# Performance work log

Measured on AMD Instinct MI355X. Metric: run time of the kernel, lower is better.

Reference implementation:

```python
import jax, jax.numpy as jnp
import numpy as np

DIM = 1024
N_HEAD = 16
N_KV_HEAD = 4
HEAD_DIM = DIM // N_HEAD  # 64
INTER = 2688
B, N = 2, 2048
EPS = 1e-6


def setup_inputs() -> dict:
    key = jax.random.key(0)
    ks = jax.random.split(key, 10)
    std = 0.02
    x = jax.random.normal(ks[0], (B, N, DIM), dtype=jnp.float32)
    # rotary embedding: theta = pos * 10000^(-2i/d), cos/sin of shape [N, HEAD_DIM//2]
    inv_freq = 1.0 / (10000.0 ** (np.arange(0, HEAD_DIM, 2, dtype=np.float32) / HEAD_DIM))
    t = np.arange(N, dtype=np.float32)
    ang = np.outer(t, inv_freq)  # [N, HEAD_DIM//2]
    rope_cos = jnp.asarray(np.cos(ang))
    rope_sin = jnp.asarray(np.sin(ang))
    mask = jnp.tril(jnp.ones((N, N), dtype=bool))  # True = attend
    return {
        "x": x,
        "w_attn_norm": jnp.ones((DIM,), jnp.float32),
        "w_ffn_norm": jnp.ones((DIM,), jnp.float32),
        "Wq": jax.random.normal(ks[1], (DIM, N_HEAD * HEAD_DIM), jnp.float32) * std,
        "Wkv": jax.random.normal(ks[2], (DIM, 2 * N_KV_HEAD * HEAD_DIM), jnp.float32) * std,
        "Wo": jax.random.normal(ks[3], (N_HEAD * HEAD_DIM, DIM), jnp.float32) * std,
        "W1": jax.random.normal(ks[4], (DIM, INTER), jnp.float32) * std,
        "W2": jax.random.normal(ks[5], (INTER, DIM), jnp.float32) * std,
        "W3": jax.random.normal(ks[6], (DIM, INTER), jnp.float32) * std,
        "rope_cos": rope_cos,
        "rope_sin": rope_sin,
        "mask": mask,
    }


def _rms_norm(x, w):
    # nn.functional.rms_norm: x / sqrt(mean(x^2) + eps) * w
    return x * jax.lax.rsqrt(jnp.mean(x * x, axis=-1, keepdims=True) + EPS) * w


def _apply_rope(x, cos, sin):
    # x: [b, n, h, d]; consecutive pairs (x[2k], x[2k+1]) form complex numbers
    xr = x[..., 0::2]
    xi = x[..., 1::2]
    c = cos[None, :, None, :]
    s = sin[None, :, None, :]
    yr = xr * c - xi * s
    yi = xr * s + xi * c
    return jnp.stack([yr, yi], axis=-1).reshape(x.shape)


def _block(x, w_attn_norm, w_ffn_norm, Wq, Wkv, Wo, W1, W2, W3, rope_cos, rope_sin, mask):
    b, n, _ = x.shape
    # --- attention (GQA, use_cache=False prefill) ---
    h = _rms_norm(x, w_attn_norm)
    q = (h @ Wq).reshape(b, n, N_HEAD, HEAD_DIM)
    kv = h @ Wkv
    k, v = jnp.split(kv, 2, axis=-1)
    k = k.reshape(b, n, N_KV_HEAD, HEAD_DIM)
    v = v.reshape(b, n, N_KV_HEAD, HEAD_DIM)
    q = _apply_rope(q, rope_cos, rope_sin)
    k = _apply_rope(k, rope_cos, rope_sin)
    # einops repeat 'b n h d -> b n (r h) d' == tile along head axis
    r = N_HEAD // N_KV_HEAD
    k = jnp.tile(k, (1, 1, r, 1))
    v = jnp.tile(v, (1, 1, r, 1))
    scale = HEAD_DIM ** -0.5
    scores = jnp.einsum('bnhd,bmhd->bhnm', q, k) * scale
    scores = jnp.where(mask[None, None, :, :], scores, jnp.finfo(scores.dtype).min)
    attn = jax.nn.softmax(scores, axis=-1)
    o = jnp.einsum('bhnm,bmhd->bnhd', attn, v).reshape(b, n, N_HEAD * HEAD_DIM)
    x = x + o @ Wo
    # --- SwiGLU MLP ---
    h2 = _rms_norm(x, w_ffn_norm)
    ff = (jax.nn.silu(h2 @ W1) * (h2 @ W3)) @ W2
    return x + ff


def reference(x, w_attn_norm, w_ffn_norm, Wq, Wkv, Wo, W1, W2, W3, rope_cos, rope_sin, mask):
    return _block(x, w_attn_norm, w_ffn_norm, Wq, Wkv, Wo, W1, W2, W3, rope_cos, rope_sin, mask)
```

## Files before the change

### kernel.cpp

```cpp
#include <hip/hip_runtime.h>

#define DIM 1024
#define NH 16
#define NKV 4
#define HD 64
#define INTER 2688
#define BB 2
#define NN 2048
#define MM (BB*NN)

typedef __attribute__((ext_vector_type(4))) float f32x4;
typedef __attribute__((ext_vector_type(16))) float f32x16;
typedef __attribute__((ext_vector_type(8))) short short8;

#define CROW(r,h) ((((r)&3)) + 8*((r)>>2) + 4*(h))

__device__ __forceinline__ unsigned short f2bf(float f) {
  union { float f; unsigned u; } v; v.f = f;
  unsigned r = v.u + 0x7fffu + ((v.u >> 16) & 1u);
  return (unsigned short)(r >> 16);
}
__device__ __forceinline__ float bf2f(unsigned short u) {
  union { unsigned u; float f; } v; v.u = ((unsigned)u) << 16; return v.f;
}
__device__ __forceinline__ float ld_res(const float* p) { return *p; }
__device__ __forceinline__ float ld_res(const unsigned short* p) { return bf2f(*p); }
__device__ __forceinline__ void st_out(float* p, float v) { *p = v; }
__device__ __forceinline__ void st_out(unsigned short* p, float v) { *p = f2bf(v); }

__device__ __forceinline__ void glds16(const unsigned short* g, unsigned short* l) {
  __builtin_amdgcn_global_load_lds(
      (const __attribute__((address_space(1))) void*)g,
      (__attribute__((address_space(3))) void*)l, 16, 0, 0);
}

__device__ __forceinline__ void xcd_map(int& bx, int& by) {
  int gx = gridDim.x;
  int nwg = gx * gridDim.y;
  int bid = (int)blockIdx.y * gx + (int)blockIdx.x;
  int cpx = nwg >> 3;
  int lg = (bid & 7) * cpx + (bid >> 3);
  bx = lg % gx;
  by = lg / gx;
}

__global__ void transpose_all(const float* __restrict__ Wq, const float* __restrict__ Wkv,
                              const float* __restrict__ Wo, const float* __restrict__ W1,
                              const float* __restrict__ W3, const float* __restrict__ W2,
                              unsigned short* __restrict__ WqkvT, unsigned short* __restrict__ WoT,
                              unsigned short* __restrict__ W1T, unsigned short* __restrict__ W3T,
                              unsigned short* __restrict__ W2T) {
  int tb = blockIdx.x;
  const float* src; unsigned short* dst; int K, Nc, t0;
  if (tb < 1024)        { src = Wq;  dst = WqkvT;                         K = 1024; Nc = 1024; t0 = tb; }
  else if (tb < 1536)   { src = Wkv; dst = WqkvT + (size_t)1024 * 1024;   K = 1024; Nc = 512;  t0 = tb - 1024; }
  else if (tb < 2560)   { src = Wo;  dst = WoT;                           K = 1024; Nc = 1024; t0 = tb - 1536; }
  else if (tb < 5248)   { src = W1;  dst = W1T;                           K = 1024; Nc = 2688; t0 = tb - 2560; }
  else if (tb < 7936)   { src = W3;  dst = W3T;                           K = 1024; Nc = 2688; t0 = tb - 5248; }
  else                  { src = W2;  dst = W2T;                           K = 2688; Nc = 1024; t0 = tb - 7936; }
  int ntx = Nc >> 5;
  int n0 = (t0 % ntx) * 32, k0 = (t0 / ntx) * 32;
  __shared__ float tile[32][33];
  int tx = threadIdx.x & 31, ty = threadIdx.x >> 5;
#pragma unroll
  for (int i = 0; i < 32; i += 8)
    tile[ty + i][tx] = src[(size_t)(k0 + ty + i) * Nc + n0 + tx];
  __syncthreads();
#pragma unroll
  for (int i = 0; i < 32; i += 8)
    dst[(size_t)(n0 + ty + i) * K + k0 + tx] = f2bf(tile[tx][ty + i]);
}

template <typename InT>
__global__ void rmsnorm_k(const InT* __restrict__ x, const float* __restrict__ w,
                          unsigned short* __restrict__ h) {
  int row = blockIdx.x;
  int t = threadIdx.x;
  float4 v;
  if constexpr (sizeof(InT) == 4) {
    v = ((const float4*)(x + (size_t)row * DIM))[t];
  } else {
    ushort4 u = ((const ushort4*)(x + (size_t)row * DIM))[t];
    v.x = bf2f(u.x); v.y = bf2f(u.y); v.z = bf2f(u.z); v.w = bf2f(u.w);
  }
  float ss = v.x * v.x + v.y * v.y + v.z * v.z + v.w * v.w;
#pragma unroll
  for (int o = 1; o < 64; o <<= 1) ss += __shfl_xor(ss, o);
  __shared__ float ps[4];
  if ((t & 63) == 0) ps[t >> 6] = ss;
  __syncthreads();
  float r = rsqrtf((ps[0] + ps[1] + ps[2] + ps[3]) * (1.0f / DIM) + 1e-6f);
  float4 wv = ((const float4*)w)[t];
  ushort4 o4;
  o4.x = f2bf(v.x * r * wv.x);
  o4.y = f2bf(v.y * r * wv.y);
  o4.z = f2bf(v.z * r * wv.z);
  o4.w = f2bf(v.w * r * wv.w);
  *(ushort4*)(h + (size_t)row * DIM + t * 4) = o4;
}

template <typename ResT, typename OutT>
__global__ __launch_bounds__(256, 3) void gemm64(
    const unsigned short* __restrict__ A, const unsigned short* __restrict__ Bt,
    const ResT* __restrict__ res, OutT* __restrict__ C, int Nc, int K) {
  __shared__ __align__(16) unsigned short Asm[2][64 * 64];
  __shared__ __align__(16) unsigned short Bsm[2][128 * 64];
  int tid = threadIdx.x;
  int w = tid >> 6, l = tid & 63;
  int bx, by;
  xcd_map(bx, by);
  int bm = by * 64, bn = bx * 128;
  int wc = w * 32;
  int c0 = l & 15, g = l >> 4;

  int sra = w * 16 + (l >> 3);
  int srb = w * 32 + (l >> 3);
  int schA = ((l & 7) ^ (l >> 3)) * 8;
  const unsigned short* gA = A + (size_t)(bm + sra) * K + schA;
  const unsigned short* gB = Bt + (size_t)(bn + srb) * K + schA;
  int lsa = (w * 16) * 64, lsb = (w * 32) * 64;

  f32x4 acc[4][2] = {};
  int T = K / 64;
  glds16(gA, &Asm[0][lsa]);
  glds16(gA + 8 * K, &Asm[0][lsa + 8 * 64]);
  glds16(gB, &Bsm[0][lsb]);
  glds16(gB + 8 * K, &Bsm[0][lsb + 8 * 64]);
  glds16(gB + 16 * K, &Bsm[0][lsb + 16 * 64]);
  glds16(gB + 24 * K, &Bsm[0][lsb + 24 * 64]);
  __syncthreads();
  int buf = 0;
  for (int s = 0; s < T; ++s) {
    int nb = buf ^ 1;
    if (s + 1 < T) {
      int ko = (s + 1) * 64;
      glds16(gA + ko, &Asm[nb][lsa]);
      glds16(gA + 8 * K + ko, &Asm[nb][lsa + 8 * 64]);
      glds16(gB + ko, &Bsm[nb][lsb]);
      glds16(gB + 8 * K + ko, &Bsm[nb][lsb + 8 * 64]);
      glds16(gB + 16 * K + ko, &Bsm[nb][lsb + 16 * 64]);
      glds16(gB + 24 * K + ko, &Bsm[nb][lsb + 24 * 64]);
    }
    const unsigned short* As = Asm[buf];
    const unsigned short* Bs = Bsm[buf];
#pragma unroll
    for (int ks = 0; ks < 2; ++ks) {
      short8 af[4], bf[2];
#pragma unroll
      for (int m = 0; m < 4; m++) {
        int ra = m * 16 + c0;
        af[m] = *(const short8*)&As[ra * 64 + (((ks * 4 + g) ^ (ra & 7)) * 8)];
      }
#pragma unroll
      for (int n = 0; n < 2; n++) {
        int rb = wc + n * 16 + c0;
        bf[n] = *(const short8*)&Bs[rb * 64 + (((ks * 4 + g) ^ (rb & 7)) * 8)];
      }
      __builtin_amdgcn_s_setprio(1);
#pragma unroll
      for (int m = 0; m < 4; m++)
#pragma unroll
        for (int n = 0; n < 2; n++)
          acc[m][n] = __builtin_amdgcn_mfma_f32_16x16x32_bf16(af[m], bf[n], acc[m][n], 0, 0, 0);
      __builtin_amdgcn_s_setprio(0);
    }
    __syncthreads();
    buf = nb;
  }
  int gq = l >> 4;
#pragma unroll
  for (int m = 0; m < 4; m++) {
#pragma unroll
    for (int i = 0; i < 4; i++) {
      int row = bm + m * 16 + gq * 4 + i;
#pragma unroll
      for (int n = 0; n < 2; n++) {
        int col = bn + wc + n * 16 + c0;
        float v = acc[m][n][i] + ld_res(&res[(size_t)row * Nc + col]);
        st_out(&C[(size_t)row * Nc + col], v);
      }
    }
  }
}

__global__ __launch_bounds__(256, 3) void gemm_qkv(
    const unsigned short* __restrict__ A, const unsigned short* __restrict__ Bt,
    const float* __restrict__ cosb, const float* __restrict__ sinb,
    unsigned short* __restrict__ qb, unsigned short* __restrict__ kb,
    unsigned short* __restrict__ vtb) {
  const int K = 1024;
  const float QS = 0.125f * 1.44269504f;
  __shared__ __align__(16) unsigned short Asm[2][64 * 64];
  __shared__ __align__(16) unsigned short Bsm[2][128 * 64];
  int tid = threadIdx.x;
  int w = tid >> 6, l = tid & 63;
  int bx, by;
  xcd_map(bx, by);
  int bm = by * 64, bn = bx * 128;
  int wc = w * 32;
  int c0 = l & 15, g = l >> 4;

  int sra = w * 16 + (l >> 3);
  int srb = w * 32 + (l >> 3);
  int schA = ((l & 7) ^ (l >> 3)) * 8;
  const unsigned short* gA = A + (size_t)(bm + sra) * K + schA;
  const unsigned short* gB = Bt + (size_t)(bn + srb) * K + schA;
  int lsa = (w * 16) * 64, lsb = (w * 32) * 64;

  f32x4 acc[4][2] = {};
  int T = K / 64;
  glds16(gA, &Asm[0][lsa]);
  glds16(gA + 8 * K, &Asm[0][lsa + 8 * 64]);
  glds16(gB, &Bsm[0][lsb]);
  glds16(gB + 8 * K, &Bsm[0][lsb + 8 * 64]);
  glds16(gB + 16 * K, &Bsm[0][lsb + 16 * 64]);
  glds16(gB + 24 * K, &Bsm[0][lsb + 24 * 64]);
  __syncthreads();
  int buf = 0;
  for (int s = 0; s < T; ++s) {
    int nb = buf ^ 1;
    if (s + 1 < T) {
      int ko = (s + 1) * 64;
      glds16(gA + ko, &Asm[nb][lsa]);
      glds16(gA + 8 * K + ko, &Asm[nb][lsa + 8 * 64]);
      glds16(gB + ko, &Bsm[nb][lsb]);
      glds16(gB + 8 * K + ko, &Bsm[nb][lsb + 8 * 64]);
      glds16(gB + 16 * K + ko, &Bsm[nb][lsb + 16 * 64]);
      glds16(gB + 24 * K + ko, &Bsm[nb][lsb + 24 * 64]);
    }
    const unsigned short* As = Asm[buf];
    const unsigned short* Bs = Bsm[buf];
#pragma unroll
    for (int ks = 0; ks < 2; ++ks) {
      short8 af[4], bf[2];
#pragma unroll
      for (int m = 0; m < 4; m++) {
        int ra = m * 16 + c0;
        af[m] = *(const short8*)&As[ra * 64 + (((ks * 4 + g) ^ (ra & 7)) * 8)];
      }
#pragma unroll
      for (int n = 0; n < 2; n++) {
        int rb = wc + n * 16 + c0;
        bf[n] = *(const short8*)&Bs[rb * 64 + (((ks * 4 + g) ^ (rb & 7)) * 8)];
      }
      __builtin_amdgcn_s_setprio(1);
#pragma unroll
      for (int m = 0; m < 4; m++)
#pragma unroll
        for (int n = 0; n < 2; n++)
          acc[m][n] = __builtin_amdgcn_mfma_f32_16x16x32_bf16(af[m], bf[n], acc[m][n], 0, 0, 0);
      __builtin_amdgcn_s_setprio(0);
    }
    __syncthreads();
    buf = nb;
  }
  int gq = l >> 4;
  int lodd = c0 & 1;
#pragma unroll
  for (int m = 0; m < 4; m++) {
#pragma unroll
    for (int i = 0; i < 4; i++) {
      int row = bm + m * 16 + gq * 4 + i;
      int b = row >> 11, tok = row & (NN - 1);
#pragma unroll
      for (int n = 0; n < 2; n++) {
        int col = bn + wc + n * 16 + c0;
        float val = acc[m][n][i];
        float partner = __shfl_xor(val, 1);
        if (bn < 1024) {
          int head = col >> 6, d = col & 63, j = d >> 1;
          float c = cosb[tok * 32 + j], s = sinb[tok * 32 + j];
          float r = lodd ? (partner * s + val * c) : (val * c - partner * s);
          qb[(((size_t)(b * NH + head)) * NN + tok) * 64 + d] = f2bf(r * QS);
        } else if (bn < 1280) {
          int cc = col - 1024;
          int kvh = cc >> 6, d = cc & 63, j = d >> 1;
          float c = cosb[tok * 32 + j], s = sinb[tok * 32 + j];
          float r = lodd ? (partner * s + val * c) : (val * c - partner * s);
          kb[(((size_t)(b * NKV + kvh)) * NN + tok) * 64 + d] = f2bf(r);
        } else {
          int cc = col - 1280;
          int kvh = cc >> 6, d = cc & 63;
          vtb[(((size_t)(b * NKV + kvh)) * 64 + d) * NN + tok] = f2bf(val);
        }
      }
    }
  }
}

__global__ __launch_bounds__(512, 2) void gemm_ffn13(
    const unsigned short* __restrict__ A, const unsigned short* __restrict__ B1t,
    const unsigned short* __restrict__ B3t, unsigned short* __restrict__ G,
    int Nc, int K) {
  __shared__ __align__(16) unsigned short Asm[3][128 * 64];
  __shared__ __align__(16) unsigned short B1sm[3][128 * 64];
  __shared__ __align__(16) unsigned short B3sm[3][128 * 64];
  int tid = threadIdx.x;
  int w = tid >> 6, l = tid & 63;
  int bid = (int)blockIdx.x;
  int xcd = bid & 7, r = bid >> 3;
  int bx = r >> 2, by = (xcd << 2) + (r & 3);
  int bm = by * 128, bn = bx * 128;
  int wm = w >> 2, wn = w & 3;
  int c0 = l & 15, g = l >> 4;

  int lr = l >> 3;
  int sch = ((l & 7) ^ lr) * 8;
  const unsigned short* gA  = A   + (size_t)(bm + w * 16 + lr) * K + sch;
  const unsigned short* gB1 = B1t + (size_t)(bn + w * 16 + lr) * K + sch;
  const unsigned short* gB3 = B3t + (size_t)(bn + w * 16 + lr) * K + sch;
  int ls = (w * 16) * 64;

  f32x4 a1[4][2] = {};
  f32x4 a3[4][2] = {};
  const int T = K / 64;

#pragma unroll
  for (int p = 0; p < 2; ++p) {
    int ko = p * 64;
    glds16(gA + ko, &Asm[p][ls]);
    glds16(gA + 8 * K + ko, &Asm[p][ls + 512]);
    glds16(gB1 + ko, &B1sm[p][ls]);
    glds16(gB1 + 8 * K + ko, &B1sm[p][ls + 512]);
    glds16(gB3 + ko, &B3sm[p][ls]);
    glds16(gB3 + 8 * K + ko, &B3sm[p][ls + 512]);
  }
  asm volatile("s_waitcnt vmcnt(6)" ::: "memory");
  asm volatile("s_barrier" ::: "memory");

  int cur = 0;
  for (int t = 0; t < T; ++t) {
    int nx = cur + 2; if (nx >= 3) nx -= 3;
    bool pre = (t + 2 < T);
    int ko = (t + 2) * 64;
    const unsigned short* As  = Asm[cur];
    const unsigned short* B1s = B1sm[cur];
    const unsigned short* B3s = B3sm[cur];
    short8 af[4], bf[2];

#pragma unroll
    for (int m = 0; m < 4; m++) {
      int ra = wm * 64 + m * 16 + c0;
      af[m] = *(const short8*)&As[ra * 64 + ((g ^ (ra & 7)) * 8)];
    }
#pragma unroll
    for (int n = 0; n < 2; n++) {
      int rb = wn * 32 + n * 16 + c0;
      bf[n] = *(const short8*)&B1s[rb * 64 + ((g ^ (rb & 7)) * 8)];
    }
    if (pre) { glds16(gA + ko, &Asm[nx][ls]); glds16(gA + 8 * K + ko, &Asm[nx][ls + 512]); }
    asm volatile("s_barrier" ::: "memory");
    asm volatile("s_waitcnt lgkmcnt(0)" ::: "memory");
    __builtin_amdgcn_sched_barrier(0);
    __builtin_amdgcn_s_setprio(1);
#pragma unroll
    for (int m = 0; m < 4; m++)
#pragma unroll
      for (int n = 0; n < 2; n++)
        a1[m][n] = __builtin_amdgcn_mfma_f32_16x16x32_bf16(af[m], bf[n], a1[m][n], 0, 0, 0);
    __builtin_amdgcn_s_setprio(0);

#pragma unroll
    for (int n = 0; n < 2; n++) {
      int rb = wn * 32 + n * 16 + c0;
      bf[n] = *(const short8*)&B3s[rb * 64 + ((g ^ (rb & 7)) * 8)];
    }
    if (pre) { glds16(gB1 + ko, &B1sm[nx][ls]); glds16(gB1 + 8 * K + ko, &B1sm[nx][ls + 512]); }
    asm volatile("s_barrier" ::: "memory");
    asm volatile("s_waitcnt lgkmcnt(0)" ::: "memory");
    __builtin_amdgcn_sched_barrier(0);
    __builtin_amdgcn_s_setprio(1);
#pragma unroll
    for (int m = 0; m < 4; m++)
#pragma unroll
      for (int n = 0; n < 2; n++)
        a3[m][n] = __builtin_amdgcn_mfma_f32_16x16x32_bf16(af[m], bf[n], a3[m][n], 0, 0, 0);
    __builtin_amdgcn_s_setprio(0);

#pragma unroll
    for (int m = 0; m < 4; m++) {
      int ra = wm * 64 + m * 16 + c0;
      af[m] = *(const short8*)&As[ra * 64 + (((4 + g) ^ (ra & 7)) * 8)];
    }
#pragma unroll
    for (int n = 0; n < 2; n++) {
      int rb = wn * 32 + n * 16 + c0;
      bf[n] = *(const short8*)&B1s[rb * 64 + (((4 + g) ^ (rb & 7)) * 8)];
    }
    if (pre) { glds16(gB3 + ko, &B3sm[nx][ls]); glds16(gB3 + 8 * K + ko, &B3sm[nx][ls + 512]); }
    asm volatile("s_barrier" ::: "memory");
    asm volatile("s_waitcnt lgkmcnt(0)" ::: "memory");
    __builtin_amdgcn_sched_barrier(0);
    __builtin_amdgcn_s_setprio(1);
#pragma unroll
    for (int m = 0; m < 4; m++)
#pragma unroll
      for (int n = 0; n < 2; n++)
        a1[m][n] = __builtin_amdgcn_mfma_f32_16x16x32_bf16(af[m], bf[n], a1[m][n], 0, 0, 0);
    __builtin_amdgcn_s_setprio(0);

#pragma unroll
    for (int n = 0; n < 2; n++) {
      int rb = wn * 32 + n * 16 + c0;
      bf[n] = *(const short8*)&B3s[rb * 64 + (((4 + g) ^ (rb & 7)) * 8)];
    }
    asm volatile("s_barrier" ::: "memory");
    asm volatile("s_waitcnt lgkmcnt(0)" ::: "memory");
    __builtin_amdgcn_sched_barrier(0);
    __builtin_amdgcn_s_setprio(1);
#pragma unroll
    for (int m = 0; m < 4; m++)
#pragma unroll
      for (int n = 0; n < 2; n++)
        a3[m][n] = __builtin_amdgcn_mfma_f32_16x16x32_bf16(af[m], bf[n], a3[m][n], 0, 0, 0);
    __builtin_amdgcn_s_setprio(0);

    if (pre) {
      asm volatile("s_waitcnt vmcnt(6)" ::: "memory");
    } else if (t + 2 == T) {
      asm volatile("s_waitcnt vmcnt(0)" ::: "memory");
    }
    if (t + 1 < T) asm volatile("s_barrier" ::: "memory");
    cur = cur + 1 == 3 ? 0 : cur + 1;
  }

  int gq = l >> 4;
#pragma unroll
  for (int m = 0; m < 4; m++) {
#pragma unroll
    for (int i = 0; i < 4; i++) {
      int row = bm + wm * 64 + m * 16 + gq * 4 + i;
#pragma unroll
      for (int n = 0; n < 2; n++) {
        int col = bn + wn * 32 + n * 16 + c0;
        float x1 = a1[m][n][i], x3 = a3[m][n][i];
        float sg = x1 / (1.0f + __expf(-x1));
        G[(size_t)row * Nc + col] = f2bf(sg * x3);
      }
    }
  }
}

__global__ __launch_bounds__(256, 3) void attn_k(
    const unsigned short* __restrict__ qg_, const unsigned short* __restrict__ kg_,
    const unsigned short* __restrict__ vg_, unsigned short* __restrict__ ob) {
  __shared__ __align__(16) unsigned short Ksm[2][64 * 64];
  __shared__ __align__(16) unsigned short Vsm[2][64 * 64];
  int qb = (blockIdx.z == 0) ? (int)blockIdx.x : ((int)gridDim.x - 1 - (int)blockIdx.x);
  int h = blockIdx.y, b = blockIdx.z;
  int kvh = h & 3;
  int tid = threadIdx.x, w = tid >> 6, l = tid & 63;
  int q5 = l & 31, hi = l >> 5;
  int qwbase = qb * 128 + w * 32;
  int qgl = qwbase + q5;

  const unsigned short* Kg = kg_ + ((size_t)(b * NKV + kvh)) * NN * 64;
  const unsigned short* Vg = vg_ + ((size_t)(b * NKV + kvh)) * 64 * NN;

  short8 qf[4];
  {
    const unsigned short* qrow = qg_ + (((size_t)(b * NH + h)) * NN + qgl) * 64 + hi * 8;
#pragma unroll
    for (int d = 0; d < 4; d++) qf[d] = *(const short8*)(qrow + d * 16);
  }

  int srow = l >> 3;
  int schunk = (l & 7) ^ (srow & 7);
  const unsigned short* gK = Kg + (size_t)(w * 16 + srow) * 64 + schunk * 8;
  const unsigned short* gV = Vg + (size_t)(w * 16 + srow) * NN + schunk * 8;

  int nkt = qb * 2 + 2;
  int nkt_w = ((qwbase + 31) >> 6) + 1;

  f32x16 O0 = {}, O1 = {};
  float m_r = -1e30f, l_r = 0.0f;

  glds16(gK, &Ksm[0][w * 1024]);
  glds16(gK + 8 * 64, &Ksm[0][w * 1024 + 512]);
  glds16(gV, &Vsm[0][w * 1024]);
  glds16(gV + 8 * NN, &Vsm[0][w * 1024 + 512]);
  __syncthreads();

  int buf = 0;
  for (int kt = 0; kt < nkt; ++kt) {
    int n0 = kt * 64;
    if (kt + 1 < nkt) {
      int nb = buf ^ 1;
      glds16(gK + (size_t)(n0 + 64) * 64, &Ksm[nb][w * 1024]);
      glds16(gK + (size_t)(n0 + 64) * 64 + 8 * 64, &Ksm[nb][w * 1024 + 512]);
      glds16(gV + n0 + 64, &Vsm[nb][w * 1024]);
      glds16(gV + 8 * NN + n0 + 64, &Vsm[nb][w * 1024 + 512]);
    }
    if (kt < nkt_w) {
      const unsigned short* Ks = Ksm[buf];
      const unsigned short* Vs = Vsm[buf];
      f32x16 S[2];
      __builtin_amdgcn_s_setprio(1);
#pragma unroll
      for (int s = 0; s < 2; s++) {
        f32x16 acc = {};
        int row = s * 32 + q5;
#pragma unroll
        for (int d = 0; d < 4; d++) {
          int ch = (2 * d + hi) ^ (row & 7);
          short8 kf = *(const short8*)&Ks[row * 64 + ch * 8];
          acc = __builtin_amdgcn_mfma_f32_32x32x16_bf16(kf, qf[d], acc, 0, 0, 0);
        }
        S[s] = acc;
      }
      __builtin_amdgcn_s_setprio(0);
      if (kt == nkt_w - 1) {
#pragma unroll
        for (int s = 0; s < 2; s++)
#pragma unroll
          for (int r = 0; r < 16; r++) {
            int kg = n0 + s * 32 + CROW(r, hi);
            S[s][r] = (kg > qgl) ? -1e30f : S[s][r];
          }
      }
      float t16[16];
#pragma unroll
      for (int r = 0; r < 16; r++) t16[r] = fmaxf(S[0][r], S[1][r]);
#pragma unroll
      for (int k = 8; k >= 1; k >>= 1)
#pragma unroll
        for (int r = 0; r < k; r++) t16[r] = fmaxf(t16[r], t16[r + k]);
      float pm = fmaxf(t16[0], __shfl_xor(t16[0], 32));
      if (!__all(pm <= m_r + 8.0f)) {
        float mn = fmaxf(m_r, pm);
        float alpha = exp2f(m_r - mn);
        m_r = mn;
        l_r *= alpha;
        float ab[16];
#pragma unroll
        for (int r = 0; r < 16; r++) ab[r] = __shfl(alpha, CROW(r, 0) + 4 * hi);
#pragma unroll
        for (int r = 0; r < 16; r++) { O0[r] *= ab[r]; O1[r] *= ab[r]; }
      }
#pragma unroll
      for (int s = 0; s < 2; s++)
#pragma unroll
        for (int r = 0; r < 16; r++) S[s][r] = exp2f(S[s][r] - m_r);
      float u[16];
#pragma unroll
      for (int r = 0; r < 16; r++) u[r] = S[0][r] + S[1][r];
#pragma unroll
      for (int k = 8; k >= 1; k >>= 1)
#pragma unroll
        for (int r = 0; r < k; r++) u[r] += u[r + k];
      l_r += (u[0] + __shfl_xor(u[0], 32));
      short8 paf[4];
#pragma unroll
      for (int ks = 0; ks < 4; ks++) {
        const int s = ks >> 1, e = ks & 1;
        unsigned a0, a1, b0, b1;
        asm("v_cvt_pk_bf16_f32 %0, %1, %2" : "=v"(a0) : "v"(S[s][8*e+0]), "v"(S[s][8*e+1]));
        asm("v_cvt_pk_bf16_f32 %0, %1, %2" : "=v"(a1) : "v"(S[s][8*e+2]), "v"(S[s][8*e+3]));
        asm("v_cvt_pk_bf16_f32 %0, %1, %2" : "=v"(b0) : "v"(S[s][8*e+4]), "v"(S[s][8*e+5]));
        asm("v_cvt_pk_bf16_f32 %0, %1, %2" : "=v"(b1) : "v"(S[s][8*e+6]), "v"(S[s][8*e+7]));
        asm("v_permlane32_swap_b32 %0, %1" : "+v"(a0), "+v"(b0));
        asm("v_permlane32_swap_b32 %0, %1" : "+v"(a1), "+v"(b1));
        union { unsigned u4[4]; short8 s8; } pk;
        pk.u4[0] = a0; pk.u4[1] = a1; pk.u4[2] = b0; pk.u4[3] = b1;
        paf[ks] = pk.s8;
      }
      __builtin_amdgcn_s_setprio(1);
#pragma unroll
      for (int ks = 0; ks < 4; ks++) {
        int row0 = q5, row1 = 32 + q5;
        short8 vf0 = *(const short8*)&Vs[row0 * 64 + (((2 * ks + hi) ^ (row0 & 7)) * 8)];
        short8 vf1 = *(const short8*)&Vs[row1 * 64 + (((2 * ks + hi) ^ (row1 & 7)) * 8)];
        O0 = __builtin_amdgcn_mfma_f32_32x32x16_bf16(paf[ks], vf0, O0, 0, 0, 0);
        O1 = __builtin_amdgcn_mfma_f32_32x32x16_bf16(paf[ks], vf1, O1, 0, 0, 0);
      }
      __builtin_amdgcn_s_setprio(0);
    }
    __syncthreads();
    buf ^= 1;
  }
  float linv = 1.0f / l_r;
  float lb[16];
#pragma unroll
  for (int r = 0; r < 16; r++) lb[r] = __shfl(linv, CROW(r, 0) + 4 * hi);
#pragma unroll
  for (int r = 0; r < 16; r++) {
    int orow = qwbase + CROW(r, hi);
    size_t base = ((size_t)b * NN + orow) * 1024 + h * 64 + q5;
    ob[base] = f2bf(O0[r] * lb[r]);
    ob[base + 32] = f2bf(O1[r] * lb[r]);
  }
}

extern "C" void kernel_launch(void* const* d_in, const int* in_sizes, int n_in,
                              void* d_out, int out_size, void* d_ws, size_t ws_size,
                              hipStream_t stream) {
  (void)in_sizes; (void)n_in; (void)out_size; (void)ws_size;
  const float* x    = (const float*)d_in[0];
  const float* w_an = (const float*)d_in[1];
  const float* w_fn = (const float*)d_in[2];
  const float* Wq   = (const float*)d_in[3];
  const float* Wkv  = (const float*)d_in[4];
  const float* Wo   = (const float*)d_in[5];
  const float* W1   = (const float*)d_in[6];
  const float* W2   = (const float*)d_in[7];
  const float* W3   = (const float*)d_in[8];
  const float* cosb = (const float*)d_in[9];
  const float* sinb = (const float*)d_in[10];
  float* out = (float*)d_out;

  char* ws = (char*)d_ws;
  size_t off = 0;
  auto take = [&](size_t bytes) {
    size_t r = off;
    off += (bytes + 255) & ~(size_t)255;
    return r;
  };
  unsigned short* WqkvT = (unsigned short*)(ws + take((size_t)1536 * 1024 * 2));
  unsigned short* WoT   = (unsigned short*)(ws + take((size_t)1024 * 1024 * 2));
  unsigned short* W1T   = (unsigned short*)(ws + take((size_t)2688 * 1024 * 2));
  unsigned short* W3T   = (unsigned short*)(ws + take((size_t)2688 * 1024 * 2));
  unsigned short* W2T   = (unsigned short*)(ws + take((size_t)2688 * 1024 * 2));
  unsigned short* hA    = (unsigned short*)(ws + take((size_t)MM * DIM * 2));
  unsigned short* gbuf  = (unsigned short*)(ws + take((size_t)MM * INTER * 2));
  unsigned short* qbuf = (unsigned short*)(ws + take((size_t)MM * DIM * 2));
  unsigned short* kbuf = (unsigned short*)(ws + take((size_t)BB * NKV * NN * HD * 2));
  unsigned short* vtb  = (unsigned short*)(ws + take((size_t)BB * NKV * NN * HD * 2));
  unsigned short* obuf = (unsigned short*)(ws + take((size_t)MM * DIM * 2));
  unsigned short* x2b  = (unsigned short*)(ws + take((size_t)MM * DIM * 2));

  transpose_all<<<10624, 256, 0, stream>>>(Wq, Wkv, Wo, W1, W3, W2,
                                           WqkvT, WoT, W1T, W3T, W2T);
  rmsnorm_k<float><<<MM, 256, 0, stream>>>(x, w_an, hA);
  gemm_qkv<<<dim3(1536 / 128, MM / 64), 256, 0, stream>>>(hA, WqkvT, cosb, sinb,
                                                          qbuf, kbuf, vtb);
  attn_k<<<dim3(NN / 128, NH, BB), 256, 0, stream>>>(qbuf, kbuf, vtb, obuf);
  gemm64<float, unsigned short><<<dim3(1024 / 128, MM / 64), 256, 0, stream>>>(
      obuf, WoT, x, x2b, 1024, 1024);
  rmsnorm_k<unsigned short><<<MM, 256, 0, stream>>>(x2b, w_fn, hA);
  gemm_ffn13<<<672, 512, 0, stream>>>(hA, W1T, W3T, gbuf, INTER, 1024);
  gemm64<unsigned short, float><<<dim3(1024 / 128, MM / 64), 256, 0, stream>>>(
      gbuf, W2T, x2b, out, 1024, 2688);
}
```

Measured before the change: 235.2 us.

## Enlarge FFN W1/W3 GEMM tile to 256x128 with double buffering

The fused W1/W3 GEMM now uses a 256x128 output tile, with 8 waves laid out 4x2, each computing 64x64 for both accumulators. The shared-memory ring drops from triple to double buffering, and the async-copy waits are rearranged to match. The XCD-aware block swizzle is replaced by a plain 2D grid. The larger tile raises arithmetic intensity per loaded byte, but it doubles the accumulator registers, shortens the prefetch lookahead, and gives fewer blocks (336 instead of 672) with possibly worse L2 locality.

```diff
diff --git a/kernel.cpp b/kernel.cpp
--- a/kernel.cpp
+++ b/kernel.cpp
@@ -292,51 +292,53 @@
     const unsigned short* __restrict__ A, const unsigned short* __restrict__ B1t,
     const unsigned short* __restrict__ B3t, unsigned short* __restrict__ G,
     int Nc, int K) {
-  __shared__ __align__(16) unsigned short Asm[3][128 * 64];
-  __shared__ __align__(16) unsigned short B1sm[3][128 * 64];
-  __shared__ __align__(16) unsigned short B3sm[3][128 * 64];
+  __shared__ __align__(16) unsigned short Asm[2][256 * 64];
+  __shared__ __align__(16) unsigned short B1sm[2][128 * 64];
+  __shared__ __align__(16) unsigned short B3sm[2][128 * 64];
   int tid = threadIdx.x;
   int w = tid >> 6, l = tid & 63;
-  int bid = (int)blockIdx.x;
-  int xcd = bid & 7, r = bid >> 3;
-  int bx = r >> 2, by = (xcd << 2) + (r & 3);
-  int bm = by * 128, bn = bx * 128;
-  int wm = w >> 2, wn = w & 3;
+  int bm = (int)blockIdx.y * 256, bn = (int)blockIdx.x * 128;
+  int wm = w >> 1, wn = w & 1;
   int c0 = l & 15, g = l >> 4;
 
   int lr = l >> 3;
   int sch = ((l & 7) ^ lr) * 8;
-  const unsigned short* gA  = A   + (size_t)(bm + w * 16 + lr) * K + sch;
-  const unsigned short* gB1 = B1t + (size_t)(bn + w * 16 + lr) * K + sch;
-  const unsigned short* gB3 = B3t + (size_t)(bn + w * 16 + lr) * K + sch;
-  int ls = (w * 16) * 64;
-
-  f32x4 a1[4][2] = {};
-  f32x4 a3[4][2] = {};
+  const unsigned short* pA0 = A + (size_t)(bm + 0 * 64 + w * 8 + lr) * K + sch;
+  const unsigned short* pA1 = A + (size_t)(bm + 1 * 64 + w * 8 + lr) * K + sch;
+  const unsigned short* pA2 = A + (size_t)(bm + 2 * 64 + w * 8 + lr) * K + sch;
+  const unsigned short* pA3 = A + (size_t)(bm + 3 * 64 + w * 8 + lr) * K + sch;
+  const unsigned short* pB1a = B1t + (size_t)(bn + w * 8 + lr) * K + sch;
+  const unsigned short* pB1b = B1t + (size_t)(bn + 64 + w * 8 + lr) * K + sch;
+  const unsigned short* pB3a = B3t + (size_t)(bn + w * 8 + lr) * K + sch;
+  const unsigned short* pB3b = B3t + (size_t)(bn + 64 + w * 8 + lr) * K + sch;
+  int lA0 = (0 * 64 + w * 8) * 64, lA1 = (1 * 64 + w * 8) * 64;
+  int lA2 = (2 * 64 + w * 8) * 64, lA3 = (3 * 64 + w * 8) * 64;
+  int lBa = (w * 8) * 64, lBb = (64 + w * 8) * 64;
+
+  f32x4 a1[4][4] = {};
+  f32x4 a3[4][4] = {};
   const int T = K / 64;
 
-#pragma unroll
-  for (int p = 0; p < 2; ++p) {
-    int ko = p * 64;
-    glds16(gA + ko, &Asm[p][ls]);
-    glds16(gA + 8 * K + ko, &Asm[p][ls + 512]);
-    glds16(gB1 + ko, &B1sm[p][ls]);
-    glds16(gB1 + 8 * K + ko, &B1sm[p][ls + 512]);
-    glds16(gB3 + ko, &B3sm[p][ls]);
-    glds16(gB3 + 8 * K + ko, &B3sm[p][ls + 512]);
-  }
-  asm volatile("s_waitcnt vmcnt(6)" ::: "memory");
-  asm volatile("s_barrier" ::: "memory");
+  glds16(pA0, &Asm[0][lA0]);
+  glds16(pA1, &Asm[0][lA1]);
+  glds16(pA2, &Asm[0][lA2]);
+  glds16(pA3, &Asm[0][lA3]);
+  glds16(pB1a, &B1sm[0][lBa]);
+  glds16(pB1b, &B1sm[0][lBb]);
+  glds16(pB3a, &B3sm[0][lBa]);
+  glds16(pB3b, &B3sm[0][lBb]);
+  asm volatile("s_waitcnt vmcnt(2)" ::: "memory");
+  __builtin_amdgcn_s_barrier();
 
   int cur = 0;
   for (int t = 0; t < T; ++t) {
-    int nx = cur + 2; if (nx >= 3) nx -= 3;
-    bool pre = (t + 2 < T);
-    int ko = (t + 2) * 64;
-    const unsigned short* As  = Asm[cur];
+    int nb = cur ^ 1;
+    bool pre = (t + 1 < T);
+    int ko = (t + 1) * 64;
+    const unsigned short* As = Asm[cur];
     const unsigned short* B1s = B1sm[cur];
     const unsigned short* B3s = B3sm[cur];
-    short8 af[4], bf[2];
+    short8 af[4], bf[4];
 
 #pragma unroll
     for (int m = 0; m < 4; m++) {
@@ -344,36 +346,68 @@
       af[m] = *(const short8*)&As[ra * 64 + ((g ^ (ra & 7)) * 8)];
     }
 #pragma unroll
-    for (int n = 0; n < 2; n++) {
-      int rb = wn * 32 + n * 16 + c0;
+    for (int n = 0; n < 4; n++) {
+      int rb = wn * 64 + n * 16 + c0;
       bf[n] = *(const short8*)&B1s[rb * 64 + ((g ^ (rb & 7)) * 8)];
     }
-    if (pre) { glds16(gA + ko, &Asm[nx][ls]); glds16(gA + 8 * K + ko, &Asm[nx][ls + 512]); }
-    asm volatile("s_barrier" ::: "memory");
+    if (pre) { glds16(pA0 + ko, &Asm[nb][lA0]); glds16(pA1 + ko, &Asm[nb][lA1]); }
+    __builtin_amdgcn_s_barrier();
     asm volatile("s_waitcnt lgkmcnt(0)" ::: "memory");
     __builtin_amdgcn_sched_barrier(0);
     __builtin_amdgcn_s_setprio(1);
 #pragma unroll
     for (int m = 0; m < 4; m++)
 #pragma unroll
-      for (int n = 0; n < 2; n++)
+      for (int n = 0; n < 4; n++)
         a1[m][n] = __builtin_amdgcn_mfma_f32_16x16x32_bf16(af[m], bf[n], a1[m][n], 0, 0, 0);
     __builtin_amdgcn_s_setprio(0);
 
 #pragma unroll
-    for (int n = 0; n < 2; n++) {
-      int rb = wn * 32 + n * 16 + c0;
-      bf[n] = *(const short8*)&B3s[rb * 64 + ((g ^ (rb & 7)) * 8)];
-    }
-    if (pre) { glds16(gB1 + ko, &B1sm[nx][ls]); glds16(gB1 + 8 * K + ko, &B1sm[nx][ls + 512]); }
-    asm volatile("s_barrier" ::: "memory");
+    for (int m = 0; m < 4; m++) {
+      int ra = wm * 64 + m * 16 + c0;
+      af[m] = *(const short8*)&As[ra * 64 + (((4 + g) ^ (ra & 7)) * 8)];
+    }
+#pragma unroll
+    for (int n = 0; n < 4; n++) {
+      int rb = wn * 64 + n * 16 + c0;
+      bf[n] = *(const short8*)&B1s[rb * 64 + (((4 + g) ^ (rb & 7)) * 8)];
+    }
+    if (pre) {
+      glds16(pA2 + ko, &Asm[nb][lA2]); glds16(pA3 + ko, &Asm[nb][lA3]);
+      asm volatile("s_waitcnt vmcnt(4)" ::: "memory");
+    } else {
+      asm volatile("s_waitcnt vmcnt(0)" ::: "memory");
+    }
+    __builtin_amdgcn_s_barrier();
     asm volatile("s_waitcnt lgkmcnt(0)" ::: "memory");
     __builtin_amdgcn_sched_barrier(0);
     __builtin_amdgcn_s_setprio(1);
 #pragma unroll
     for (int m = 0; m < 4; m++)
 #pragma unroll
-      for (int n = 0; n < 2; n++)
+      for (int n = 0; n < 4; n++)
+        a1[m][n] = __builtin_amdgcn_mfma_f32_16x16x32_bf16(af[m], bf[n], a1[m][n], 0, 0, 0);
+    __builtin_amdgcn_s_setprio(0);
+
+#pragma unroll
+    for (int m = 0; m < 4; m++) {
+      int ra = wm * 64 + m * 16 + c0;
+      af[m] = *(const short8*)&As[ra * 64 + ((g ^ (ra & 7)) * 8)];
+    }
+#pragma unroll
+    for (int n = 0; n < 4; n++) {
+      int rb = wn * 64 + n * 16 + c0;
+      bf[n] = *(const short8*)&B3s[rb * 64 + ((g ^ (rb & 7)) * 8)];
+    }
+    if (pre) { glds16(pB1a + ko, &B1sm[nb][lBa]); glds16(pB1b + ko, &B1sm[nb][lBb]); }
+    __builtin_amdgcn_s_barrier();
+    asm volatile("s_waitcnt lgkmcnt(0)" ::: "memory");
+    __builtin_amdgcn_sched_barrier(0);
+    __builtin_amdgcn_s_setprio(1);
+#pragma unroll
+    for (int m = 0; m < 4; m++)
+#pragma unroll
+      for (int n = 0; n < 4; n++)
         a3[m][n] = __builtin_amdgcn_mfma_f32_16x16x32_bf16(af[m], bf[n], a3[m][n], 0, 0, 0);
     __builtin_amdgcn_s_setprio(0);
 
@@ -383,45 +417,26 @@
       af[m] = *(const short8*)&As[ra * 64 + (((4 + g) ^ (ra & 7)) * 8)];
     }
 #pragma unroll
-    for (int n = 0; n < 2; n++) {
-      int rb = wn * 32 + n * 16 + c0;
-      bf[n] = *(const short8*)&B1s[rb * 64 + (((4 + g) ^ (rb & 7)) * 8)];
-    }
-    if (pre) { glds16(gB3 + ko, &B3sm[nx][ls]); glds16(gB3 + 8 * K + ko, &B3sm[nx][ls + 512]); }
-    asm volatile("s_barrier" ::: "memory");
+    for (int n = 0; n < 4; n++) {
+      int rb = wn * 64 + n * 16 + c0;
+      bf[n] = *(const short8*)&B3s[rb * 64 + (((4 + g) ^ (rb & 7)) * 8)];
+    }
+    if (pre) {
+      glds16(pB3a + ko, &B3sm[nb][lBa]); glds16(pB3b + ko, &B3sm[nb][lBb]);
+      asm volatile("s_waitcnt vmcnt(2)" ::: "memory");
+    }
+    __builtin_amdgcn_s_barrier();
     asm volatile("s_waitcnt lgkmcnt(0)" ::: "memory");
     __builtin_amdgcn_sched_barrier(0);
     __builtin_amdgcn_s_setprio(1);
 #pragma unroll
     for (int m = 0; m < 4; m++)
 #pragma unroll
-      for (int n = 0; n < 2; n++)
-        a1[m][n] = __builtin_amdgcn_mfma_f32_16x16x32_bf16(af[m], bf[n], a1[m][n], 0, 0, 0);
-    __builtin_amdgcn_s_setprio(0);
-
-#pragma unroll
-    for (int n = 0; n < 2; n++) {
-      int rb = wn * 32 + n * 16 + c0;
-      bf[n] = *(const short8*)&B3s[rb * 64 + (((4 + g) ^ (rb & 7)) * 8)];
-    }
-    asm volatile("s_barrier" ::: "memory");
-    asm volatile("s_waitcnt lgkmcnt(0)" ::: "memory");
-    __builtin_amdgcn_sched_barrier(0);
-    __builtin_amdgcn_s_setprio(1);
-#pragma unroll
-    for (int m = 0; m < 4; m++)
-#pragma unroll
-      for (int n = 0; n < 2; n++)
+      for (int n = 0; n < 4; n++)
         a3[m][n] = __builtin_amdgcn_mfma_f32_16x16x32_bf16(af[m], bf[n], a3[m][n], 0, 0, 0);
     __builtin_amdgcn_s_setprio(0);
 
-    if (pre) {
-      asm volatile("s_waitcnt vmcnt(6)" ::: "memory");
-    } else if (t + 2 == T) {
-      asm volatile("s_waitcnt vmcnt(0)" ::: "memory");
-    }
-    if (t + 1 < T) asm volatile("s_barrier" ::: "memory");
-    cur = cur + 1 == 3 ? 0 : cur + 1;
+    cur = nb;
   }
 
   int gq = l >> 4;
@@ -431,8 +446,8 @@
     for (int i = 0; i < 4; i++) {
       int row = bm + wm * 64 + m * 16 + gq * 4 + i;
 #pragma unroll
-      for (int n = 0; n < 2; n++) {
-        int col = bn + wn * 32 + n * 16 + c0;
+      for (int n = 0; n < 4; n++) {
+        int col = bn + wn * 64 + n * 16 + c0;
         float x1 = a1[m][n][i], x3 = a3[m][n][i];
         float sg = x1 / (1.0f + __expf(-x1));
         G[(size_t)row * Nc + col] = f2bf(sg * x3);
@@ -637,7 +652,7 @@
   gemm64<float, unsigned short><<<dim3(1024 / 128, MM / 64), 256, 0, stream>>>(
       obuf, WoT, x, x2b, 1024, 1024);
   rmsnorm_k<unsigned short><<<MM, 256, 0, stream>>>(x2b, w_fn, hA);
-  gemm_ffn13<<<672, 512, 0, stream>>>(hA, W1T, W3T, gbuf, INTER, 1024);
+  gemm_ffn13<<<dim3(INTER / 128, MM / 256), 512, 0, stream>>>(hA, W1T, W3T, gbuf, INTER, 1024);
   gemm64<unsigned short, float><<<dim3(1024 / 128, MM / 64), 256, 0, stream>>>(
       gbuf, W2T, x2b, out, 1024, 2688);
 }
```

After: 228.6 us. 2.8% less time.
